# Optimization experiments

Measured on AMD Instinct MI355X. Metric: run time of the kernel, lower is better.

The kernel has to match this reference:

```python
import jax, jax.numpy as jnp
import numpy as np

N = 100000          # num nodes
E = 1600000         # num edges
EMB = 192           # embedding_dimension (divisible by 3)
THIRD = EMB // 3    # 64
NUM_REL = 2
SLOPE = 0.01        # LeakyReLU default negative slope


def leaky_relu(x):
    return jnp.where(x >= 0, x, SLOPE * x)


def setup_inputs() -> dict:
    key = jax.random.key(0)
    ks = jax.random.split(key, 20)
    s = 0.02
    inp = {
        "des": jax.random.normal(ks[0], (N, 768), jnp.float32),
        "tweet": jax.random.normal(ks[1], (N, 768), jnp.float32),
        "num_prop": jax.random.normal(ks[2], (N, 4), jnp.float32),
        "cat_prop": jax.random.normal(ks[3], (N, 3), jnp.float32),
        "edge_index": jax.random.randint(ks[4], (2, E), 0, N, jnp.int64).astype(jnp.int32),
        "edge_type": jax.random.randint(ks[5], (E,), 0, NUM_REL, jnp.int32),
        # params
        "W_des": s * jax.random.normal(ks[6], (768, THIRD), jnp.float32),
        "b_des": jnp.zeros((THIRD,), jnp.float32),
        "W_num": s * jax.random.normal(ks[7], (4, THIRD), jnp.float32),
        "b_num": jnp.zeros((THIRD,), jnp.float32),
        "W_cat": s * jax.random.normal(ks[8], (3, THIRD), jnp.float32),
        "b_cat": jnp.zeros((THIRD,), jnp.float32),
        "W_in": s * jax.random.normal(ks[9], (EMB, EMB), jnp.float32),
        "b_in": jnp.zeros((EMB,), jnp.float32),
        "W_root": s * jax.random.normal(ks[10], (EMB, EMB), jnp.float32),
        "W_rel": s * jax.random.normal(ks[11], (NUM_REL, EMB, EMB), jnp.float32),
        "b_rgcn": jnp.zeros((EMB,), jnp.float32),
        "W_o1": s * jax.random.normal(ks[12], (EMB, EMB), jnp.float32),
        "b_o1": jnp.zeros((EMB,), jnp.float32),
        "W_o2": s * jax.random.normal(ks[13], (EMB, 2), jnp.float32),
        "b_o2": jnp.zeros((2,), jnp.float32),
    }
    return inp


def rgcn_conv(x, edge_index, edge_type, W_root, W_rel, b_rgcn):
    # PyG RGCNConv (default): out = x @ W_root + b + sum_r mean_{edges r -> i}(x[src] @ W_r)
    # mean of (x_j @ W_r) == (mean of x_j) @ W_r, so aggregate first (cheaper).
    src, dst = edge_index[0], edge_index[1]
    h = x[src]  # [E, EMB] gather
    out = x @ W_root + b_rgcn
    for r in range(NUM_REL):
        m = (edge_type == r).astype(x.dtype)  # [E]
        s = jax.ops.segment_sum(h * m[:, None], dst, num_segments=N)  # [N, EMB]
        cnt = jax.ops.segment_sum(m, dst, num_segments=N)             # [N]
        agg = s / jnp.maximum(cnt, 1.0)[:, None]
        out = out + agg @ W_rel[r]
    return out


def reference(des, tweet, num_prop, cat_prop, edge_index, edge_type,
              W_des, b_des, W_num, b_num, W_cat, b_cat, W_in, b_in,
              W_root, W_rel, b_rgcn, W_o1, b_o1, W_o2, b_o2):
    d = leaky_relu(des @ W_des + b_des)
    n = leaky_relu(num_prop @ W_num + b_num)
    c = leaky_relu(cat_prop @ W_cat + b_cat)
    x = jnp.concatenate((d, n, c), axis=1)          # [N, EMB]
    x = leaky_relu(x @ W_in + b_in)
    x = rgcn_conv(x, edge_index, edge_type, W_root, W_rel, b_rgcn)
    # dropout in eval mode = identity
    x = rgcn_conv(x, edge_index, edge_type, W_root, W_rel, b_rgcn)
    x = leaky_relu(x @ W_o1 + b_o1)
    x = x @ W_o2 + b_o2                              # [N, 2]
    return x
```

## Files before the change

### kernel.cpp

```cpp
#include <hip/hip_runtime.h>

typedef _Float16 f16;
typedef _Float16 f16x4 __attribute__((ext_vector_type(4)));
typedef _Float16 f16x8 __attribute__((ext_vector_type(8)));
typedef float f32x4 __attribute__((ext_vector_type(4)));

#define LRELU(v) ((v) >= 0.f ? (v) : 0.01f * (v))

__device__ __forceinline__ int swz(int a) { return a ^ (((a >> 7) & 7) << 4); }

__device__ __forceinline__ f16x4 shflx4(f16x4 v, int m) {
  union { f16x4 h; int i[2]; } u;
  u.h = v;
  u.i[0] = __shfl_xor(u.i[0], m);
  u.i[1] = __shfl_xor(u.i[1], m);
  return u.h;
}

#define BCAP 64

__global__ __launch_bounds__(256) void setup_kernel(
    const float* __restrict__ num_prop, const float* __restrict__ cat_prop,
    const float* __restrict__ W_num, const float* __restrict__ b_num,
    const float* __restrict__ W_cat, const float* __restrict__ b_cat,
    const float* __restrict__ W_des, const float* __restrict__ W_in,
    const float* __restrict__ W_root, const float* __restrict__ W_rel,
    const float* __restrict__ W_o1,
    f16* __restrict__ x0, int* __restrict__ cursor,
    f16* __restrict__ WtDes, f16* __restrict__ WtIn, f16* __restrict__ WtR,
    f16* __restrict__ WtO1,
    int N, int nbf, int nbz)
{
  int b = blockIdx.x;
  int tid = threadIdx.x;
  if (b < nbf) {
    int w = (b * 256 + tid) >> 6;
    int lane = tid & 63;
    if (w < N) {
      const float* npr = num_prop + (size_t)w * 4;
      const float* cpr = cat_prop + (size_t)w * 3;
      float vn = b_num[lane];
#pragma unroll
      for (int k = 0; k < 4; k++) vn += npr[k] * W_num[k * 64 + lane];
      float vc = b_cat[lane];
#pragma unroll
      for (int k = 0; k < 3; k++) vc += cpr[k] * W_cat[k * 64 + lane];
      vn = LRELU(vn);
      vc = LRELU(vc);
      x0[(size_t)w * 192 + 64 + lane] = (f16)vn;
      x0[(size_t)w * 192 + 128 + lane] = (f16)vc;
    }
    return;
  }
  b -= nbf;
  if (b < nbz) {
    int i = b * 256 + tid;
    if (i < N) cursor[i] = 0;
    return;
  }
  b -= nbz;
  if (b < 192) {
    int idx = b * 256 + tid;
    if (idx < 64 * 768) { int n = idx / 768, k = idx % 768; WtDes[idx] = (f16)W_des[k * 64 + n]; }
    return;
  }
  b -= 192;
  if (b < 144) {
    int idx = b * 256 + tid;
    if (idx < 192 * 192) { int n = idx / 192, k = idx % 192; WtIn[idx] = (f16)W_in[k * 192 + n]; }
    return;
  }
  b -= 144;
  if (b < 432) {
    int idx = b * 256 + tid;
    if (idx < 192 * 576) {
      int n = idx / 576, k = idx % 576;
      int seg = k / 192, kk = k % 192;
      float v = (seg == 0) ? W_root[kk * 192 + n] : W_rel[(seg - 1) * 192 * 192 + kk * 192 + n];
      WtR[idx] = (f16)v;
    }
    return;
  }
  b -= 432;
  {
    int idx = b * 256 + tid;
    if (idx < 192 * 192) { int n = idx / 192, k = idx % 192; WtO1[idx] = (f16)W_o1[k * 192 + n]; }
  }
}

__global__ __launch_bounds__(256) void cfdes_kernel(
    const float* __restrict__ A, const f16* __restrict__ Bt,
    const float* __restrict__ bias, f16* __restrict__ C, int M,
    const int* __restrict__ ei, const int* __restrict__ et,
    int* __restrict__ cursor, int* __restrict__ bucket, int E, int nbDES)
{
  __shared__ f16 lA[128 * 64];
  __shared__ f16 lB[64 * 64];
  if ((int)blockIdx.x >= nbDES) {
    int e = ((int)blockIdx.x - nbDES) * 256 + threadIdx.x;
    if (e < E) {
      int src = ei[e];
      int dst = ei[E + e];
      int r = et[e];
      int pos = atomicAdd(&cursor[dst], 1);
      if (pos < BCAP) bucket[(size_t)dst * BCAP + pos] = src | (r << 31);
    }
    return;
  }
  const int tid = threadIdx.x, lane = tid & 63, wid = tid >> 6;
  const int wm = wid >> 1, wn = wid & 1;
  const int m0 = blockIdx.x * 128;
  f32x4 acc[4][2] = {};
  const int arow = tid >> 1, ahalf = tid & 1;
  int agr = m0 + arow;
  if (agr >= M) agr = M - 1;
  const float* asrc = A + (size_t)agr * 768 + ahalf * 32;
  for (int k0 = 0; k0 < 768; k0 += 64) {
    {
      const float4* s4 = reinterpret_cast<const float4*>(asrc + k0);
#pragma unroll
      for (int i = 0; i < 4; i++) {
        float4 u = s4[2 * i], w = s4[2 * i + 1];
        f16x8 h;
        h[0] = (f16)u.x; h[1] = (f16)u.y; h[2] = (f16)u.z; h[3] = (f16)u.w;
        h[4] = (f16)w.x; h[5] = (f16)w.y; h[6] = (f16)w.z; h[7] = (f16)w.w;
        int boff = arow * 128 + ahalf * 64 + i * 16;
        *reinterpret_cast<f16x8*>((char*)lA + swz(boff)) = h;
      }
    }
    {
#pragma unroll
      for (int i = 0; i < 2; i++) {
        int c = tid + i * 256;
        int n = c >> 3, k8 = c & 7;
        f16x8 h = *reinterpret_cast<const f16x8*>(Bt + (size_t)n * 768 + k0 + k8 * 8);
        *reinterpret_cast<f16x8*>((char*)lB + swz(n * 128 + k8 * 16)) = h;
      }
    }
    __syncthreads();
#pragma unroll
    for (int ks = 0; ks < 2; ks++) {
      f16x8 af[4], bf[2];
#pragma unroll
      for (int fm = 0; fm < 4; fm++) {
        int row = wm * 64 + fm * 16 + (lane & 15);
        af[fm] = *reinterpret_cast<const f16x8*>((const char*)lA + swz(row * 128 + ks * 64 + (lane >> 4) * 16));
      }
#pragma unroll
      for (int fn = 0; fn < 2; fn++) {
        int nn = wn * 32 + fn * 16 + (lane & 15);
        bf[fn] = *reinterpret_cast<const f16x8*>((const char*)lB + swz(nn * 128 + ks * 64 + (lane >> 4) * 16));
      }
#pragma unroll
      for (int fm = 0; fm < 4; fm++)
#pragma unroll
        for (int fn = 0; fn < 2; fn++)
          acc[fm][fn] = __builtin_amdgcn_mfma_f32_16x16x32_f16(af[fm], bf[fn], acc[fm][fn], 0, 0, 0);
    }
    __syncthreads();
  }
#pragma unroll
  for (int fm = 0; fm < 4; fm++) {
#pragma unroll
    for (int fn = 0; fn < 2; fn++) {
      int gc = wn * 32 + fn * 16 + (lane & 15);
      float b = bias[gc];
#pragma unroll
      for (int r = 0; r < 4; r++) {
        int gr = m0 + wm * 64 + fm * 16 + (lane >> 4) * 4 + r;
        if (gr < M) {
          float v = acc[fm][fn][r] + b;
          C[(size_t)gr * 192 + gc] = (f16)LRELU(v);
        }
      }
    }
  }
}

template <int NSEG, bool RELU, bool OUT2>
__global__ __launch_bounds__(512) void gemm_x_kernel(
    const f16* __restrict__ A0, const f16* __restrict__ A1, const f16* __restrict__ A2,
    const f16* __restrict__ Bt, const float* __restrict__ bias,
    f16* __restrict__ C, int M,
    const float* __restrict__ W_o2, const float* __restrict__ b_o2,
    float* __restrict__ out)
{
  __shared__ f16 lA[128 * 64];
  __shared__ f16 lB[192 * 64];
  const int tid = threadIdx.x, lane = tid & 63, wid = tid >> 6;
  const int wm = wid >> 2, wn = wid & 3;
  const int m0 = blockIdx.x * 128;
  const int Ktot = NSEG * 192;
  f32x4 acc[4][3] = {};
  const f16* segs[3] = {A0, A1, A2};
  const int arow = tid >> 2, aq = tid & 3;
  int agr = m0 + arow;
  if (agr >= M) agr = M - 1;
  int seg = 0, kin = 0;
  for (int it = 0; it < NSEG * 3; it++) {
    {
      const f16x8* s8 = reinterpret_cast<const f16x8*>(segs[seg] + (size_t)agr * 192 + kin + aq * 16);
      f16x8 h0 = s8[0], h1 = s8[1];
      int b0 = arow * 128 + aq * 32;
      *reinterpret_cast<f16x8*>((char*)lA + swz(b0)) = h0;
      *reinterpret_cast<f16x8*>((char*)lA + swz(b0 + 16)) = h1;
    }
    {
      int kb = it * 64;
#pragma unroll
      for (int i = 0; i < 3; i++) {
        int c = tid + i * 512;
        int n = c >> 3, k8 = c & 7;
        f16x8 h = *reinterpret_cast<const f16x8*>(Bt + (size_t)n * Ktot + kb + k8 * 8);
        *reinterpret_cast<f16x8*>((char*)lB + swz(n * 128 + k8 * 16)) = h;
      }
    }
    __syncthreads();
#pragma unroll
    for (int ks = 0; ks < 2; ks++) {
      f16x8 af[4], bf[3];
#pragma unroll
      for (int fm = 0; fm < 4; fm++) {
        int row = wm * 64 + fm * 16 + (lane & 15);
        af[fm] = *reinterpret_cast<const f16x8*>((const char*)lA + swz(row * 128 + ks * 64 + (lane >> 4) * 16));
      }
#pragma unroll
      for (int fn = 0; fn < 3; fn++) {
        int nn = wn * 48 + fn * 16 + (lane & 15);
        bf[fn] = *reinterpret_cast<const f16x8*>((const char*)lB + swz(nn * 128 + ks * 64 + (lane >> 4) * 16));
      }
#pragma unroll
      for (int fm = 0; fm < 4; fm++)
#pragma unroll
        for (int fn = 0; fn < 3; fn++)
          acc[fm][fn] = __builtin_amdgcn_mfma_f32_16x16x32_f16(af[fm], bf[fn], acc[fm][fn], 0, 0, 0);
    }
    __syncthreads();
    kin += 64;
    if (kin == 192) { kin = 0; if (seg < NSEG - 1) seg++; }
  }
  if (OUT2) {
    __shared__ float red[128][2];
    for (int i = tid; i < 256; i += 512) ((float*)red)[i] = 0.f;
    __syncthreads();
    float bb[3], w2v[3][2];
#pragma unroll
    for (int fn = 0; fn < 3; fn++) {
      int gc = wn * 48 + fn * 16 + (lane & 15);
      bb[fn] = bias[gc];
      w2v[fn][0] = W_o2[gc * 2 + 0];
      w2v[fn][1] = W_o2[gc * 2 + 1];
    }
#pragma unroll
    for (int fm = 0; fm < 4; fm++) {
#pragma unroll
      for (int r = 0; r < 4; r++) {
        float p0 = 0.f, p1 = 0.f;
#pragma unroll
        for (int fn = 0; fn < 3; fn++) {
          float v = acc[fm][fn][r] + bb[fn];
          v = LRELU(v);
          p0 += v * w2v[fn][0];
          p1 += v * w2v[fn][1];
        }
#pragma unroll
        for (int m = 1; m < 16; m <<= 1) { p0 += __shfl_xor(p0, m); p1 += __shfl_xor(p1, m); }
        if ((lane & 15) == 0) {
          int lr = wm * 64 + fm * 16 + (lane >> 4) * 4 + r;
          atomicAdd(&red[lr][0], p0);
          atomicAdd(&red[lr][1], p1);
        }
      }
    }
    __syncthreads();
    if (tid < 256) {
      int gr = m0 + (tid >> 1);
      if (gr < M) out[(size_t)gr * 2 + (tid & 1)] = red[tid >> 1][tid & 1] + b_o2[tid & 1];
    }
  } else {
#pragma unroll
    for (int fm = 0; fm < 4; fm++) {
#pragma unroll
      for (int fn = 0; fn < 3; fn++) {
        int gc = wn * 48 + fn * 16 + (lane & 15);
        float b = bias[gc];
#pragma unroll
        for (int r = 0; r < 4; r++) {
          int gr = m0 + wm * 64 + fm * 16 + (lane >> 4) * 4 + r;
          if (gr < M) {
            float v = acc[fm][fn][r] + b;
            if (RELU) v = LRELU(v);
            C[(size_t)gr * 192 + gc] = (f16)v;
          }
        }
      }
    }
  }
}

__global__ __launch_bounds__(256) void agg_kernel(
    const f16* __restrict__ x, const int* __restrict__ bucket,
    const int* __restrict__ cursor,
    f16* __restrict__ agg0, f16* __restrict__ agg1, int N)
{
  int w = (blockIdx.x << 2) + (threadIdx.x >> 6);
  if (w >= N) return;
  const int lane = threadIdx.x & 63;
  const int g = lane >> 4, sub = lane & 15;
  int deg = cursor[w];
  if (deg > BCAP) deg = BCAP;
  const int4* bk4 = reinterpret_cast<const int4*>(bucket + (size_t)w * BCAP);
  f16x4 a0[3] = {}, a1[3] = {};
  float c1f = 0.f;
  int nj = (deg + 15) >> 4;
  for (int j = 0; j < nj; ++j) {
    int4 ee = bk4[j * 4 + g];
#pragma unroll
    for (int i = 0; i < 4; ++i) {
      int idx = j * 16 + g * 4 + i;
      if (idx < deg) {
        int e = (i == 0) ? ee.x : (i == 1) ? ee.y : (i == 2) ? ee.z : ee.w;
        int src = e & 0x7fffffff;
        const f16* rowp = x + (size_t)src * 192 + sub * 4;
        f16x4 v0 = *reinterpret_cast<const f16x4*>(rowp);
        f16x4 v1 = *reinterpret_cast<const f16x4*>(rowp + 64);
        f16x4 v2 = *reinterpret_cast<const f16x4*>(rowp + 128);
        if (e < 0) {
          c1f += 1.f;
          a1[0] += v0; a1[1] += v1; a1[2] += v2;
        } else {
          a0[0] += v0; a0[1] += v1; a0[2] += v2;
        }
      }
    }
  }
#pragma unroll
  for (int c = 0; c < 3; ++c) {
    a0[c] += shflx4(a0[c], 16); a0[c] += shflx4(a0[c], 32);
    a1[c] += shflx4(a1[c], 16); a1[c] += shflx4(a1[c], 32);
  }
  c1f += __shfl_xor(c1f, 16); c1f += __shfl_xor(c1f, 32);
  if (g == 0) {
    float c0f = (float)deg - c1f;
    float i0 = 1.f / fmaxf(c0f, 1.f);
    float i1 = 1.f / fmaxf(c1f, 1.f);
#pragma unroll
    for (int c = 0; c < 3; ++c) {
      f16x4 o0, o1;
#pragma unroll
      for (int k = 0; k < 4; ++k) {
        o0[k] = (f16)((float)a0[c][k] * i0);
        o1[k] = (f16)((float)a1[c][k] * i1);
      }
      *reinterpret_cast<f16x4*>(agg0 + (size_t)w * 192 + c * 64 + sub * 4) = o0;
      *reinterpret_cast<f16x4*>(agg1 + (size_t)w * 192 + c * 64 + sub * 4) = o1;
    }
  }
}

extern "C" void kernel_launch(void* const* d_in, const int* in_sizes, int n_in,
                              void* d_out, int out_size, void* d_ws, size_t ws_size,
                              hipStream_t stream)
{
  const float* des      = (const float*)d_in[0];
  const float* num_prop = (const float*)d_in[2];
  const float* cat_prop = (const float*)d_in[3];
  const int* edge_index = (const int*)d_in[4];
  const int* edge_type  = (const int*)d_in[5];
  const float* W_des = (const float*)d_in[6];
  const float* b_des = (const float*)d_in[7];
  const float* W_num = (const float*)d_in[8];
  const float* b_num = (const float*)d_in[9];
  const float* W_cat = (const float*)d_in[10];
  const float* b_cat = (const float*)d_in[11];
  const float* W_in  = (const float*)d_in[12];
  const float* b_in  = (const float*)d_in[13];
  const float* W_root= (const float*)d_in[14];
  const float* W_rel = (const float*)d_in[15];
  const float* b_rgcn= (const float*)d_in[16];
  const float* W_o1  = (const float*)d_in[17];
  const float* b_o1  = (const float*)d_in[18];
  const float* W_o2  = (const float*)d_in[19];
  const float* b_o2  = (const float*)d_in[20];
  float* out = (float*)d_out;

  const int N = in_sizes[2] / 4;
  const int E = in_sizes[5];
  (void)n_in; (void)out_size; (void)ws_size;

  char* base = (char*)d_ws;
  size_t off = 0;
  auto take = [&](size_t bytes) -> void* {
    void* p = base + off;
    off += (bytes + 255) & ~(size_t)255;
    return p;
  };
  f16* xA     = (f16*)take((size_t)N * 192 * 2);
  f16* xB     = (f16*)take((size_t)N * 192 * 2);
  f16* agg0   = (f16*)take((size_t)N * 192 * 2);
  f16* agg1   = (f16*)take((size_t)N * 192 * 2);
  int* bucket = (int*)take((size_t)N * BCAP * 4);
  int* cursor = (int*)take((size_t)N * 4);
  f16* WtDes  = (f16*)take(64 * 768 * 2);
  f16* WtIn   = (f16*)take(192 * 192 * 2);
  f16* WtR    = (f16*)take(192 * 576 * 2);
  f16* WtO1   = (f16*)take(192 * 192 * 2);

  const int nbf = (N + 3) / 4;
  const int nbz = (N + 255) / 256;
  const int nsetup = nbf + nbz + 192 + 144 + 432 + 144;
  setup_kernel<<<nsetup, 256, 0, stream>>>(
      num_prop, cat_prop, W_num, b_num, W_cat, b_cat,
      W_des, W_in, W_root, W_rel, W_o1,
      xA, cursor, WtDes, WtIn, WtR, WtO1, N, nbf, nbz);
  const int nbDES = (N + 127) / 128;
  const int nbCF = (E + 255) / 256;
  cfdes_kernel<<<nbDES + nbCF, 256, 0, stream>>>(
      des, WtDes, b_des, xA, N, edge_index, edge_type, cursor, bucket, E, nbDES);
  gemm_x_kernel<1, true, false><<<(N + 127) / 128, 512, 0, stream>>>(
      xA, xA, xA, WtIn, b_in, xB, N, nullptr, nullptr, nullptr);
  agg_kernel<<<(N + 3) / 4, 256, 0, stream>>>(xB, bucket, cursor, agg0, agg1, N);
  gemm_x_kernel<3, false, false><<<(N + 127) / 128, 512, 0, stream>>>(
      xB, agg0, agg1, WtR, b_rgcn, xA, N, nullptr, nullptr, nullptr);
  agg_kernel<<<(N + 3) / 4, 256, 0, stream>>>(xA, bucket, cursor, agg0, agg1, N);
  gemm_x_kernel<3, false, false><<<(N + 127) / 128, 512, 0, stream>>>(
      xA, agg0, agg1, WtR, b_rgcn, xB, N, nullptr, nullptr, nullptr);
  gemm_x_kernel<1, false, true><<<(N + 127) / 128, 512, 0, stream>>>(
      xB, xB, xB, WtO1, b_o1, nullptr, N, W_o2, b_o2, out);
}
```

Baseline: 487.8 us.

## Replace global-atomic edge bucketing with two-level counting sort by destination bin

Edges are no longer bucketed with one global atomicAdd per edge on a per-destination cursor. A per-tile histogram over 256-node bins, a single-block scan and a scatter into a coarse-sorted array come first, then each bin does its fine bucketing with LDS atomics, fused into the des GEMM launch. This is meant to remove contended global atomics and scattered bucket writes. It adds three extra launches, a serial single-block scan, and packing that assumes node ids fit in 17 bits and fewer than 512 bins.

```diff
diff --git a/kernel.cpp b/kernel.cpp
--- a/kernel.cpp
+++ b/kernel.cpp
@@ -18,6 +18,7 @@
 }
 
 #define BCAP 64
+#define TILE 4096
 
 __global__ __launch_bounds__(256) void setup_kernel(
     const float* __restrict__ num_prop, const float* __restrict__ cat_prop,
@@ -26,10 +27,10 @@
     const float* __restrict__ W_des, const float* __restrict__ W_in,
     const float* __restrict__ W_root, const float* __restrict__ W_rel,
     const float* __restrict__ W_o1,
-    f16* __restrict__ x0, int* __restrict__ cursor,
+    f16* __restrict__ x0,
     f16* __restrict__ WtDes, f16* __restrict__ WtIn, f16* __restrict__ WtR,
     f16* __restrict__ WtO1,
-    int N, int nbf, int nbz)
+    int N, int nbf)
 {
   int b = blockIdx.x;
   int tid = threadIdx.x;
@@ -53,12 +54,6 @@
     return;
   }
   b -= nbf;
-  if (b < nbz) {
-    int i = b * 256 + tid;
-    if (i < N) cursor[i] = 0;
-    return;
-  }
-  b -= nbz;
   if (b < 192) {
     int idx = b * 256 + tid;
     if (idx < 64 * 768) { int n = idx / 768, k = idx % 768; WtDes[idx] = (f16)W_des[k * 64 + n]; }
@@ -88,26 +83,107 @@
   }
 }
 
-__global__ __launch_bounds__(256) void cfdes_kernel(
-    const float* __restrict__ A, const f16* __restrict__ Bt,
-    const float* __restrict__ bias, f16* __restrict__ C, int M,
+__global__ __launch_bounds__(256) void hist_kernel(
+    const int* __restrict__ ei, int* __restrict__ hist, int E, int NB)
+{
+  __shared__ int h[512];
+  const int tid = threadIdx.x;
+  for (int i = tid; i < NB; i += 256) h[i] = 0;
+  __syncthreads();
+  const int base = blockIdx.x * TILE;
+#pragma unroll
+  for (int i = 0; i < TILE / 256; ++i) {
+    int e = base + i * 256 + tid;
+    if (e < E) atomicAdd(&h[ei[E + e] >> 8], 1);
+  }
+  __syncthreads();
+  for (int i = tid; i < NB; i += 256) hist[blockIdx.x * NB + i] = h[i];
+}
+
+__global__ __launch_bounds__(512) void scan_kernel(
+    int* __restrict__ hist, int* __restrict__ binbase, int NB, int NBLK)
+{
+  __shared__ int s[512];
+  const int b = threadIdx.x;
+  int total = 0;
+  if (b < NB) {
+#pragma unroll 8
+    for (int blk = 0; blk < NBLK; ++blk) total += hist[blk * NB + b];
+  }
+  s[b] = total;
+  __syncthreads();
+  for (int off = 1; off < 512; off <<= 1) {
+    int v = (b >= off) ? s[b - off] : 0;
+    __syncthreads();
+    s[b] += v;
+    __syncthreads();
+  }
+  int ex = (b == 0) ? 0 : s[b - 1];
+  if (b < NB) binbase[b] = ex;
+  if (b == 0) binbase[NB] = s[511];
+  if (b < NB) {
+    int run = ex;
+#pragma unroll 8
+    for (int blk = 0; blk < NBLK; ++blk) {
+      int t = hist[blk * NB + b];
+      hist[blk * NB + b] = run;
+      run += t;
+    }
+  }
+}
+
+__global__ __launch_bounds__(256) void scatter_kernel(
     const int* __restrict__ ei, const int* __restrict__ et,
-    int* __restrict__ cursor, int* __restrict__ bucket, int E, int nbDES)
-{
-  __shared__ f16 lA[128 * 64];
-  __shared__ f16 lB[64 * 64];
-  if ((int)blockIdx.x >= nbDES) {
-    int e = ((int)blockIdx.x - nbDES) * 256 + threadIdx.x;
+    const int* __restrict__ hist, int* __restrict__ sorted, int E, int NB)
+{
+  __shared__ int cur[512];
+  const int tid = threadIdx.x;
+  for (int i = tid; i < NB; i += 256) cur[i] = hist[blockIdx.x * NB + i];
+  __syncthreads();
+  const int base = blockIdx.x * TILE;
+#pragma unroll
+  for (int i = 0; i < TILE / 256; ++i) {
+    int e = base + i * 256 + tid;
     if (e < E) {
       int src = ei[e];
       int dst = ei[E + e];
       int r = et[e];
-      int pos = atomicAdd(&cursor[dst], 1);
-      if (pos < BCAP) bucket[(size_t)dst * BCAP + pos] = src | (r << 31);
-    }
+      int slot = atomicAdd(&cur[dst >> 8], 1);
+      sorted[slot] = src | (r << 17) | ((dst & 255) << 18);
+    }
+  }
+}
+
+__global__ __launch_bounds__(256) void finedes_kernel(
+    const float* __restrict__ A, const f16* __restrict__ Bt,
+    const float* __restrict__ bias, f16* __restrict__ C, int M,
+    const int* __restrict__ sorted, const int* __restrict__ binbase,
+    int* __restrict__ bucket, int* __restrict__ cursor, int nbDES)
+{
+  __shared__ f16 lA[128 * 64];
+  __shared__ f16 lB[64 * 64];
+  const int tid = threadIdx.x;
+  if ((int)blockIdx.x >= nbDES) {
+    int bb = (int)blockIdx.x - nbDES;
+    int* cur = (int*)lA;
+    cur[tid] = 0;
+    __syncthreads();
+    int start = binbase[bb], end = binbase[bb + 1];
+    for (int j = start + tid; j < end; j += 256) {
+      int it = sorted[j];
+      int dl = (it >> 18) & 255;
+      int pos = atomicAdd(&cur[dl], 1);
+      if (pos < BCAP) {
+        int val = (it & 0x1FFFF) | (int)(((unsigned)(it >> 17) & 1u) << 31);
+        bucket[(((size_t)(bb << 8) + dl) << 6) + pos] = val;
+      }
+    }
+    __syncthreads();
+    int dst = (bb << 8) + tid;
+    if (dst < M) cursor[dst] = cur[tid];
     return;
   }
-  const int tid = threadIdx.x, lane = tid & 63, wid = tid >> 6;
+  const int lane = tid & 63, wid = tid >> 6;
   const int wm = wid >> 1, wn = wid & 1;
   const int m0 = blockIdx.x * 128;
   f32x4 acc[4][2] = {};
@@ -388,6 +464,9 @@
   const int E = in_sizes[5];
   (void)n_in; (void)out_size; (void)ws_size;
 
+  const int NB = (N + 255) >> 8;
+  const int NBLK = (E + TILE - 1) / TILE;
+
   char* base = (char*)d_ws;
   size_t off = 0;
   auto take = [&](size_t bytes) -> void* {
@@ -395,28 +474,32 @@
     off += (bytes + 255) & ~(size_t)255;
     return p;
   };
-  f16* xA     = (f16*)take((size_t)N * 192 * 2);
-  f16* xB     = (f16*)take((size_t)N * 192 * 2);
-  f16* agg0   = (f16*)take((size_t)N * 192 * 2);
-  f16* agg1   = (f16*)take((size_t)N * 192 * 2);
-  int* bucket = (int*)take((size_t)N * BCAP * 4);
-  int* cursor = (int*)take((size_t)N * 4);
-  f16* WtDes  = (f16*)take(64 * 768 * 2);
-  f16* WtIn   = (f16*)take(192 * 192 * 2);
-  f16* WtR    = (f16*)take(192 * 576 * 2);
-  f16* WtO1   = (f16*)take(192 * 192 * 2);
+  f16* xA      = (f16*)take((size_t)N * 192 * 2);
+  f16* xB      = (f16*)take((size_t)N * 192 * 2);
+  f16* agg0    = (f16*)take((size_t)N * 192 * 2);
+  f16* agg1    = (f16*)take((size_t)N * 192 * 2);
+  int* bucket  = (int*)take((size_t)N * BCAP * 4);
+  int* cursor  = (int*)take((size_t)N * 4);
+  int* sorted  = (int*)take((size_t)E * 4);
+  int* hist    = (int*)take((size_t)NBLK * NB * 4);
+  int* binbase = (int*)take((size_t)(NB + 2) * 4);
+  f16* WtDes   = (f16*)take(64 * 768 * 2);
+  f16* WtIn    = (f16*)take(192 * 192 * 2);
+  f16* WtR     = (f16*)take(192 * 576 * 2);
+  f16* WtO1    = (f16*)take(192 * 192 * 2);
 
   const int nbf = (N + 3) / 4;
-  const int nbz = (N + 255) / 256;
-  const int nsetup = nbf + nbz + 192 + 144 + 432 + 144;
+  const int nsetup = nbf + 192 + 144 + 432 + 144;
   setup_kernel<<<nsetup, 256, 0, stream>>>(
       num_prop, cat_prop, W_num, b_num, W_cat, b_cat,
       W_des, W_in, W_root, W_rel, W_o1,
-      xA, cursor, WtDes, WtIn, WtR, WtO1, N, nbf, nbz);
+      xA, WtDes, WtIn, WtR, WtO1, N, nbf);
+  hist_kernel<<<NBLK, 256, 0, stream>>>(edge_index, hist, E, NB);
+  scan_kernel<<<1, 512, 0, stream>>>(hist, binbase, NB, NBLK);
+  scatter_kernel<<<NBLK, 256, 0, stream>>>(edge_index, edge_type, hist, sorted, E, NB);
   const int nbDES = (N + 127) / 128;
-  const int nbCF = (E + 255) / 256;
-  cfdes_kernel<<<nbDES + nbCF, 256, 0, stream>>>(
-      des, WtDes, b_des, xA, N, edge_index, edge_type, cursor, bucket, E, nbDES);
+  finedes_kernel<<<nbDES + NB, 256, 0, stream>>>(
+      des, WtDes, b_des, xA, N, sorted, binbase, bucket, cursor, nbDES);
   gemm_x_kernel<1, true, false><<<(N + 127) / 128, 512, 0, stream>>>(
       xA, xA, xA, WtIn, b_in, xB, N, nullptr, nullptr, nullptr);
   agg_kernel<<<(N + 3) / 4, 256, 0, stream>>>(xB, bucket, cursor, agg0, agg1, N);
```

After: 541.8 us. +11.1%, slower.
